# Kernel optimization log

Hardware: AMD Instinct MI355X
Metric: run time of the kernel (lower is better)

## Reference

```python
import jax, jax.numpy as jnp
import numpy as np

KS = 7       # neighborhood kernel size (fixed in __init__)
HEADS = 8    # num_heads (fixed in __init__)
LN_EPS = 1e-5


def _nbr_idx(L, k):
    # NATTEN-style clamped window: window start shifts inward at borders (no padding)
    starts = jnp.clip(jnp.arange(L) - k // 2, 0, L - k)
    idx = starts[:, None] + jnp.arange(k)            # [L, k] absolute neighbor coords
    rel = idx - jnp.arange(L)[:, None] + (k - 1)     # [L, k] rel-pos-bias index in [0, 2k-2]
    return idx, rel


def _na2d(x, qkv_w, qkv_b, proj_w, proj_b, rpb):
    # x: [B, H, W, C]  -> neighborhood attention with clamped 7x7 windows
    B, H, W, C = x.shape
    hd = C // HEADS
    qkv = x @ qkv_w.T + qkv_b                        # [B,H,W,3C]
    q, k, v = jnp.split(qkv, 3, axis=-1)
    q = q.reshape(B, H, W, HEADS, hd) * (hd ** -0.5)
    k = k.reshape(B, H, W, HEADS, hd)
    v = v.reshape(B, H, W, HEADS, hd)
    ri, rri = _nbr_idx(H, KS)                        # [H,KS]
    ci, rci = _nbr_idx(W, KS)                        # [W,KS]
    # gather neighborhoods: [B,H,W,KS,KS,heads,hd]
    kn = k[:, ri[:, None, :, None], ci[None, :, None, :]]
    vn = v[:, ri[:, None, :, None], ci[None, :, None, :]]
    scores = jnp.einsum('bijhd,bijpqhd->bhijpq', q, kn)   # [B,heads,H,W,KS,KS]
    bias = rpb[:, rri[:, None, :, None], rci[None, :, None, :]]  # [heads,H,W,KS,KS]
    scores = scores + bias[None]
    attn = jax.nn.softmax(scores.reshape(B, HEADS, H, W, KS * KS), axis=-1)
    vn = vn.reshape(B, H, W, KS * KS, HEADS, hd)
    out = jnp.einsum('bhijp,bijphd->bijhd', attn, vn)      # [B,H,W,heads,hd]
    out = out.reshape(B, H, W, C)
    return out @ proj_w.T + proj_b


def _layernorm(x, g, b):
    mu = jnp.mean(x, axis=-1, keepdims=True)
    var = jnp.mean((x - mu) ** 2, axis=-1, keepdims=True)
    return (x - mu) * jax.lax.rsqrt(var + LN_EPS) * g + b


def setup_inputs() -> dict:
    key = jax.random.key(0)
    ks = jax.random.split(key, 4)
    B, T, H, W, C = 2, 8, 48, 48, 64
    return {
        'q': jax.random.normal(ks[0], (B, T, H, W, C), dtype=jnp.float32),
        'qkv_w': jax.random.normal(ks[1], (3 * C, C), dtype=jnp.float32) * 0.02,
        'qkv_b': jnp.zeros((3 * C,), jnp.float32),
        'proj_w': jax.random.normal(ks[2], (C, C), dtype=jnp.float32) * 0.02,
        'proj_b': jnp.zeros((C,), jnp.float32),
        'rpb': jax.random.normal(ks[3], (HEADS, 2 * KS - 1, 2 * KS - 1), dtype=jnp.float32) * 0.02,
        'ln_g': jnp.ones((C,), jnp.float32),
        'ln_b': jnp.zeros((C,), jnp.float32),
    }


def reference(q, qkv_w, qkv_b, proj_w, proj_b, rpb, ln_g, ln_b):
    B, T, H, W, C = q.shape
    x = q.reshape(B * T, H, W, C)                    # '(b t) h w c'
    x = _na2d(x, qkv_w, qkv_b, proj_w, proj_b, rpb)  # wPT path
    x = x.reshape(B, T, H, W, C)
    return _layernorm(x, ln_g, ln_b)                 # norm_q; wGC=False
```

## Files before the change

### kernel.cpp

```cpp
#include <hip/hip_runtime.h>
#include <hip/hip_bf16.h>

#define BT   16
#define IH   48
#define IW   48
#define CH   64
#define NH   8
#define HD   8
#define KS   7
#define NPIX (BT*IH*IW)
#define QKVC 192
#define LN_EPS 1e-5f
#define QSCALE 0.35355339059327373f

#define TS   8
#define HS   14
#define HP   (HS*HS)
#define KVS  136
#define AOS  72
#define RPBN (NH*(2*KS-1)*(2*KS-1))

typedef __bf16 bf16_t;
typedef bf16_t bf16x8 __attribute__((ext_vector_type(8)));
typedef float  f32x4  __attribute__((ext_vector_type(4)));

__device__ __forceinline__ float bflo(unsigned u) { union { unsigned i; float f; } v; v.i = u << 16; return v.f; }
__device__ __forceinline__ float bfhi(unsigned u) { union { unsigned i; float f; } v; v.i = u & 0xffff0000u; return v.f; }

__device__ __forceinline__ void ld8bf(const __hip_bfloat16* p, float f[8]) {
    uint4 u = *reinterpret_cast<const uint4*>(p);
    f[0] = bflo(u.x); f[1] = bfhi(u.x);
    f[2] = bflo(u.y); f[3] = bfhi(u.y);
    f[4] = bflo(u.z); f[5] = bfhi(u.z);
    f[6] = bflo(u.w); f[7] = bfhi(u.w);
}

__device__ __forceinline__ void unp8(uint4 u, float f[8]) {
    f[0] = bflo(u.x); f[1] = bfhi(u.x);
    f[2] = bflo(u.y); f[3] = bfhi(u.y);
    f[4] = bflo(u.z); f[5] = bfhi(u.z);
    f[6] = bflo(u.w); f[7] = bfhi(u.w);
}

__device__ __forceinline__ bf16x8 pack_bf16x8(float4 lo, float4 hi) {
    bf16x8 r;
    r[0] = (bf16_t)lo.x; r[1] = (bf16_t)lo.y; r[2] = (bf16_t)lo.z; r[3] = (bf16_t)lo.w;
    r[4] = (bf16_t)hi.x; r[5] = (bf16_t)hi.y; r[6] = (bf16_t)hi.z; r[7] = (bf16_t)hi.w;
    return r;
}

__global__ __launch_bounds__(256) void qkv_kernel(
        const float* __restrict__ x,
        const float* __restrict__ w,
        const float* __restrict__ b,
        __hip_bfloat16* __restrict__ qkv) {
    const int gw   = blockIdx.x * 4 + (threadIdx.x >> 6);
    const int ngrp = gw % 3;
    const int mg   = gw / 3;
    const int l  = threadIdx.x & 63;
    const int m  = l & 15;
    const int kg = l >> 4;

    const int ch_base = ngrp * 64 + m * 4;
    const float4 bias4 = *(const float4*)(b + ch_base);
    const float scale = (ngrp == 0) ? QSCALE : 1.f;

    bf16x8 wb0[4], wb1[4];
    #pragma unroll
    for (int t = 0; t < 4; ++t) {
        const float* wr_ = w + (size_t)(ch_base + t) * CH + kg * 8;
        wb0[t] = pack_bf16x8(*(const float4*)(wr_),      *(const float4*)(wr_ + 4));
        wb1[t] = pack_bf16x8(*(const float4*)(wr_ + 32), *(const float4*)(wr_ + 36));
    }

    #pragma unroll
    for (int mm = 0; mm < 2; ++mm) {
        const int mtile = mg * 2 + mm;
        const float* xr = x + (size_t)(mtile * 16 + m) * CH + kg * 8;
        const bf16x8 a0 = pack_bf16x8(*(const float4*)(xr),      *(const float4*)(xr + 4));
        const bf16x8 a1 = pack_bf16x8(*(const float4*)(xr + 32), *(const float4*)(xr + 36));

        float val[4][4];
        #pragma unroll
        for (int t = 0; t < 4; ++t) {
            f32x4 acc = {0.f, 0.f, 0.f, 0.f};
            acc = __builtin_amdgcn_mfma_f32_16x16x32_bf16(a0, wb0[t], acc, 0, 0, 0);
            acc = __builtin_amdgcn_mfma_f32_16x16x32_bf16(a1, wb1[t], acc, 0, 0, 0);
            const float bias = (t == 0) ? bias4.x : (t == 1) ? bias4.y : (t == 2) ? bias4.z : bias4.w;
            #pragma unroll
            for (int r = 0; r < 4; ++r) val[t][r] = (acc[r] + bias) * scale;
        }
        #pragma unroll
        for (int r = 0; r < 4; ++r) {
            const int pix = mtile * 16 + kg * 4 + r;
            union { ushort4 u; __hip_bfloat16 hh[4]; } pk;
            #pragma unroll
            for (int t = 0; t < 4; ++t) pk.hh[t] = __float2bfloat16(val[t][r]);
            *reinterpret_cast<ushort4*>(qkv + (size_t)pix * QKVC + ch_base) = pk.u;
        }
    }
}

__global__ __launch_bounds__(512, 4) void attn_proj_ln_kernel(
        const __hip_bfloat16* __restrict__ qkv,
        const float* __restrict__ rpb,
        const float* __restrict__ pw,
        const float* __restrict__ pb,
        const float* __restrict__ g,
        const float* __restrict__ beta,
        float* __restrict__ out) {
    __shared__ __align__(16) __hip_bfloat16 kv[HP * KVS];
    __shared__ __align__(16) __hip_bfloat16 ao[TS * TS * AOS];
    __shared__ float rpbs[RPBN];

    const int blk = blockIdx.x;
    const int n   = blk / 36;
    const int t2  = blk % 36;
    const int i0  = (t2 / 6) * TS;
    const int j0  = (t2 % 6) * TS;
    const int tid = threadIdx.x;
    const size_t img = (size_t)n * (IH * IW);

    for (int idx = tid; idx < RPBN; idx += 512) rpbs[idx] = rpb[idx];
    for (int c = tid; c < HP * 16; c += 512) {
        const int px = c >> 4, part = c & 15;
        const int hr = px / HS, hc = px - hr * HS;
        int gr = i0 - 3 + hr; gr = gr < 0 ? 0 : (gr > IH - 1 ? IH - 1 : gr);
        int gc = j0 - 3 + hc; gc = gc < 0 ? 0 : (gc > IW - 1 ? IW - 1 : gc);
        const uint4 v = *reinterpret_cast<const uint4*>(
            qkv + (img + gr * IW + gc) * QKVC + CH + part * 8);
        *reinterpret_cast<uint4*>(kv + px * KVS + part * 8) = v;
    }
    __syncthreads();

    {
        const int h  = tid & 7;
        const int pl = tid >> 3;
        const int i  = i0 + (pl >> 3);
        const int j  = j0 + (pl & 7);

        float qv[HD];
        ld8bf(qkv + (img + i * IW + j) * QKVC + h * HD, qv);

        int si = i - 3; si = si < 0 ? 0 : (si > IH - KS ? IH - KS : si);
        int sj = j - 3; sj = sj < 0 ? 0 : (sj > IW - KS ? IW - KS : sj);
        const float* rp = rpbs + h * (2*KS-1) * (2*KS-1) + (sj - j + (KS - 1));
        const int hjb = sj - (j0 - 3);

        float lrun = 0.f;
        float acc[HD];
        #pragma unroll
        for (int d = 0; d < HD; ++d) acc[d] = 0.f;

        for (int p = 0; p < KS; ++p) {
            const int ki = si + p;
            const float* rprow = rp + (ki - i + (KS - 1)) * (2*KS-1);
            const __hip_bfloat16* row = kv + ((ki - (i0 - 3)) * HS + hjb) * KVS + h * HD;

            uint4 kb[KS], vb[KS];
            #pragma unroll
            for (int qq = 0; qq < KS; ++qq) {
                kb[qq] = *reinterpret_cast<const uint4*>(row + qq * KVS);
                vb[qq] = *reinterpret_cast<const uint4*>(row + qq * KVS + CH);
            }
            float e[KS];
            #pragma unroll
            for (int qq = 0; qq < KS; ++qq) {
                float kf[HD];
                unp8(kb[qq], kf);
                float sc = rprow[qq];
                #pragma unroll
                for (int d = 0; d < HD; ++d) sc += qv[d] * kf[d];
                e[qq] = __expf(sc);
            }
            #pragma unroll
            for (int qq = 0; qq < KS; ++qq) {
                lrun += e[qq];
                float vf[HD];
                unp8(vb[qq], vf);
                #pragma unroll
                for (int d = 0; d < HD; ++d) acc[d] += e[qq] * vf[d];
            }
        }
        const float inv = 1.f / lrun;
        union { uint4 u; __hip_bfloat16 hh[8]; } pk;
        #pragma unroll
        for (int d = 0; d < HD; ++d) pk.hh[d] = __float2bfloat16(acc[d] * inv);
        *reinterpret_cast<uint4*>(ao + pl * AOS + h * HD) = pk.u;
    }
    __syncthreads();

    const int wv = tid >> 6;
    if (wv < 4) {
        const int l  = tid & 63;
        const int m  = l & 15;
        const int kg = l >> 4;

        const __hip_bfloat16* ar = ao + (wv * 16 + m) * AOS + kg * 8;
        const bf16x8 a0 = *reinterpret_cast<const bf16x8*>(ar);
        const bf16x8 a1 = *reinterpret_cast<const bf16x8*>(ar + 32);

        const int ch_base = m * 4;
        const float4 bias4 = *(const float4*)(pb + ch_base);

        float val[4][4];
        #pragma unroll
        for (int t = 0; t < 4; ++t) {
            const float* wr_ = pw + (size_t)(ch_base + t) * CH + kg * 8;
            const bf16x8 b0 = pack_bf16x8(*(const float4*)(wr_),      *(const float4*)(wr_ + 4));
            const bf16x8 b1 = pack_bf16x8(*(const float4*)(wr_ + 32), *(const float4*)(wr_ + 36));
            f32x4 acc = {0.f, 0.f, 0.f, 0.f};
            acc = __builtin_amdgcn_mfma_f32_16x16x32_bf16(a0, b0, acc, 0, 0, 0);
            acc = __builtin_amdgcn_mfma_f32_16x16x32_bf16(a1, b1, acc, 0, 0, 0);
            const float bias = (t == 0) ? bias4.x : (t == 1) ? bias4.y : (t == 2) ? bias4.z : bias4.w;
            #pragma unroll
            for (int r = 0; r < 4; ++r) val[t][r] = acc[r] + bias;
        }

        float sm[4];
        #pragma unroll
        for (int r = 0; r < 4; ++r) sm[r] = val[0][r] + val[1][r] + val[2][r] + val[3][r];
        #pragma unroll
        for (int mask = 1; mask <= 8; mask <<= 1) {
            #pragma unroll
            for (int r = 0; r < 4; ++r) sm[r] += __shfl_xor(sm[r], mask, 64);
        }
        float mu[4];
        #pragma unroll
        for (int r = 0; r < 4; ++r) mu[r] = sm[r] * (1.f / 64.f);

        float qs[4];
        #pragma unroll
        for (int r = 0; r < 4; ++r) {
            float a = val[0][r] - mu[r], bq = val[1][r] - mu[r];
            float c = val[2][r] - mu[r], d = val[3][r] - mu[r];
            qs[r] = a * a + bq * bq + c * c + d * d;
        }
        #pragma unroll
        for (int mask = 1; mask <= 8; mask <<= 1) {
            #pragma unroll
            for (int r = 0; r < 4; ++r) qs[r] += __shfl_xor(qs[r], mask, 64);
        }
        float rs[4];
        #pragma unroll
        for (int r = 0; r < 4; ++r) rs[r] = rsqrtf(qs[r] * (1.f / 64.f) + LN_EPS);

        const float4 g4  = *(const float4*)(g + ch_base);
        const float4 be4 = *(const float4*)(beta + ch_base);
        #pragma unroll
        for (int r = 0; r < 4; ++r) {
            const int pl = wv * 16 + kg * 4 + r;
            const int gi = i0 + (pl >> 3), gj = j0 + (pl & 7);
            float4 o;
            o.x = (val[0][r] - mu[r]) * rs[r] * g4.x + be4.x;
            o.y = (val[1][r] - mu[r]) * rs[r] * g4.y + be4.y;
            o.z = (val[2][r] - mu[r]) * rs[r] * g4.z + be4.z;
            o.w = (val[3][r] - mu[r]) * rs[r] * g4.w + be4.w;
            *reinterpret_cast<float4*>(out + (img + gi * IW + gj) * CH + ch_base) = o;
        }
    }
}

extern "C" void kernel_launch(void* const* d_in, const int* in_sizes, int n_in,
                              void* d_out, int out_size, void* d_ws, size_t ws_size,
                              hipStream_t stream) {
    const float* x      = (const float*)d_in[0];
    const float* qkv_w  = (const float*)d_in[1];
    const float* qkv_b  = (const float*)d_in[2];
    const float* proj_w = (const float*)d_in[3];
    const float* proj_b = (const float*)d_in[4];
    const float* rpb    = (const float*)d_in[5];
    const float* ln_g   = (const float*)d_in[6];
    const float* ln_b   = (const float*)d_in[7];
    float* out = (float*)d_out;

    __hip_bfloat16* qkv = (__hip_bfloat16*)d_ws;

    qkv_kernel<<<864, 256, 0, stream>>>(x, qkv_w, qkv_b, qkv);
    attn_proj_ln_kernel<<<576, 512, 0, stream>>>(qkv, rpb, proj_w, proj_b,
                                                 ln_g, ln_b, out);
}
```

Before: 120.3 us.

## Split fused attention+proj+LN into separate kernels reading K/V directly from global

The fused attention/projection/layernorm kernel becomes two kernels. The attention kernel drops the LDS halo staging and reads K/V and the relative-position bias straight from global memory (through cache), using 256-thread 4x8 tiles and packed f32x2 math. A separate proj+LN kernel reads a bf16 intermediate from the workspace. This removes the LDS footprint and barriers to raise occupancy, at the cost of an extra kernel launch, an intermediate round-trip through memory, and uncached-in-LDS repeated neighbor loads.

After: 120.8 us. About the same (+0.4%).

```diff
diff --git a/kernel.cpp b/kernel.cpp
--- a/kernel.cpp
+++ b/kernel.cpp
@@ -13,34 +13,14 @@
 #define LN_EPS 1e-5f
 #define QSCALE 0.35355339059327373f
 
-#define TS   8
-#define HS   14
-#define HP   (HS*HS)
-#define KVS  136
-#define AOS  72
-#define RPBN (NH*(2*KS-1)*(2*KS-1))
-
 typedef __bf16 bf16_t;
 typedef bf16_t bf16x8 __attribute__((ext_vector_type(8)));
 typedef float  f32x4  __attribute__((ext_vector_type(4)));
+typedef float  f32x2  __attribute__((ext_vector_type(2)));
 
 __device__ __forceinline__ float bflo(unsigned u) { union { unsigned i; float f; } v; v.i = u << 16; return v.f; }
 __device__ __forceinline__ float bfhi(unsigned u) { union { unsigned i; float f; } v; v.i = u & 0xffff0000u; return v.f; }
-
-__device__ __forceinline__ void ld8bf(const __hip_bfloat16* p, float f[8]) {
-    uint4 u = *reinterpret_cast<const uint4*>(p);
-    f[0] = bflo(u.x); f[1] = bfhi(u.x);
-    f[2] = bflo(u.y); f[3] = bfhi(u.y);
-    f[4] = bflo(u.z); f[5] = bfhi(u.z);
-    f[6] = bflo(u.w); f[7] = bfhi(u.w);
-}
-
-__device__ __forceinline__ void unp8(uint4 u, float f[8]) {
-    f[0] = bflo(u.x); f[1] = bfhi(u.x);
-    f[2] = bflo(u.y); f[3] = bfhi(u.y);
-    f[4] = bflo(u.z); f[5] = bfhi(u.z);
-    f[6] = bflo(u.w); f[7] = bfhi(u.w);
-}
+__device__ __forceinline__ f32x2 unp2(unsigned u) { f32x2 r; r.x = bflo(u); r.y = bfhi(u); return r; }
 
 __device__ __forceinline__ bf16x8 pack_bf16x8(float4 lo, float4 hi) {
     bf16x8 r;
@@ -101,163 +81,154 @@
     }
 }
 
-__global__ __launch_bounds__(512, 4) void attn_proj_ln_kernel(
+__global__ __launch_bounds__(256, 8) void attn_kernel(
         const __hip_bfloat16* __restrict__ qkv,
         const float* __restrict__ rpb,
+        __hip_bfloat16* __restrict__ aout) {
+    const int blk  = blockIdx.x;
+    const int n    = blk & 15;
+    const int tile = blk >> 4;
+    const int i0   = (tile / 6) * 4;
+    const int j0   = (tile % 6) * 8;
+    const int tid  = threadIdx.x;
+    const int h    = tid & 7;
+    const int pl   = tid >> 3;
+    const int i    = i0 + (pl >> 3);
+    const int j    = j0 + (pl & 7);
+    const size_t img = (size_t)n * (IH * IW);
+
+    f32x2 qv[4];
+    {
+        const uint4 u = *reinterpret_cast<const uint4*>(
+            qkv + (img + i * IW + j) * QKVC + h * HD);
+        qv[0] = unp2(u.x); qv[1] = unp2(u.y); qv[2] = unp2(u.z); qv[3] = unp2(u.w);
+    }
+
+    int si = i - 3; si = si < 0 ? 0 : (si > IH - KS ? IH - KS : si);
+    int sj = j - 3; sj = sj < 0 ? 0 : (sj > IW - KS ? IW - KS : sj);
+    const float* rp = rpb + h * (2*KS-1) * (2*KS-1) + (sj - j + (KS - 1));
+
+    float lrun = 0.f;
+    f32x2 acc[4];
+    #pragma unroll
+    for (int d = 0; d < 4; ++d) acc[d] = (f32x2){0.f, 0.f};
+
+    for (int p = 0; p < KS; ++p) {
+        const int ki = si + p;
+        const float* rprow = rp + (ki - i + (KS - 1)) * (2*KS-1);
+        const __hip_bfloat16* row = qkv + (img + ki * IW + sj) * QKVC + CH + h * HD;
+
+        uint4 kb[KS];
+        float rb[KS];
+        #pragma unroll
+        for (int qq = 0; qq < KS; ++qq) {
+            kb[qq] = *reinterpret_cast<const uint4*>(row + qq * QKVC);
+            rb[qq] = rprow[qq];
+        }
+        float e[KS];
+        #pragma unroll
+        for (int qq = 0; qq < KS; ++qq) {
+            f32x2 s2 = qv[0] * unp2(kb[qq].x);
+            s2 += qv[1] * unp2(kb[qq].y);
+            s2 += qv[2] * unp2(kb[qq].z);
+            s2 += qv[3] * unp2(kb[qq].w);
+            e[qq] = __expf(s2.x + s2.y + rb[qq]);
+        }
+        uint4 vb[KS];
+        #pragma unroll
+        for (int qq = 0; qq < KS; ++qq)
+            vb[qq] = *reinterpret_cast<const uint4*>(row + qq * QKVC + CH);
+        #pragma unroll
+        for (int qq = 0; qq < KS; ++qq) {
+            lrun += e[qq];
+            acc[0] += e[qq] * unp2(vb[qq].x);
+            acc[1] += e[qq] * unp2(vb[qq].y);
+            acc[2] += e[qq] * unp2(vb[qq].z);
+            acc[3] += e[qq] * unp2(vb[qq].w);
+        }
+    }
+    const float inv = 1.f / lrun;
+    union { uint4 u; __hip_bfloat16 hh[8]; } pk;
+    #pragma unroll
+    for (int d = 0; d < 4; ++d) {
+        pk.hh[2*d]   = __float2bfloat16(acc[d].x * inv);
+        pk.hh[2*d+1] = __float2bfloat16(acc[d].y * inv);
+    }
+    *reinterpret_cast<uint4*>(aout + (img + i * IW + j) * CH + h * HD) = pk.u;
+}
+
+__global__ __launch_bounds__(256) void proj_ln_kernel(
+        const __hip_bfloat16* __restrict__ aout,
         const float* __restrict__ pw,
         const float* __restrict__ pb,
         const float* __restrict__ g,
         const float* __restrict__ beta,
         float* __restrict__ out) {
-    __shared__ __align__(16) __hip_bfloat16 kv[HP * KVS];
-    __shared__ __align__(16) __hip_bfloat16 ao[TS * TS * AOS];
-    __shared__ float rpbs[RPBN];
-
-    const int blk = blockIdx.x;
-    const int n   = blk / 36;
-    const int t2  = blk % 36;
-    const int i0  = (t2 / 6) * TS;
-    const int j0  = (t2 % 6) * TS;
-    const int tid = threadIdx.x;
-    const size_t img = (size_t)n * (IH * IW);
-
-    for (int idx = tid; idx < RPBN; idx += 512) rpbs[idx] = rpb[idx];
-    for (int c = tid; c < HP * 16; c += 512) {
-        const int px = c >> 4, part = c & 15;
-        const int hr = px / HS, hc = px - hr * HS;
-        int gr = i0 - 3 + hr; gr = gr < 0 ? 0 : (gr > IH - 1 ? IH - 1 : gr);
-        int gc = j0 - 3 + hc; gc = gc < 0 ? 0 : (gc > IW - 1 ? IW - 1 : gc);
-        const uint4 v = *reinterpret_cast<const uint4*>(
-            qkv + (img + gr * IW + gc) * QKVC + CH + part * 8);
-        *reinterpret_cast<uint4*>(kv + px * KVS + part * 8) = v;
-    }
-    __syncthreads();
-
-    {
-        const int h  = tid & 7;
-        const int pl = tid >> 3;
-        const int i  = i0 + (pl >> 3);
-        const int j  = j0 + (pl & 7);
-
-        float qv[HD];
-        ld8bf(qkv + (img + i * IW + j) * QKVC + h * HD, qv);
-
-        int si = i - 3; si = si < 0 ? 0 : (si > IH - KS ? IH - KS : si);
-        int sj = j - 3; sj = sj < 0 ? 0 : (sj > IW - KS ? IW - KS : sj);
-        const float* rp = rpbs + h * (2*KS-1) * (2*KS-1) + (sj - j + (KS - 1));
-        const int hjb = sj - (j0 - 3);
-
-        float lrun = 0.f;
-        float acc[HD];
-        #pragma unroll
-        for (int d = 0; d < HD; ++d) acc[d] = 0.f;
-
-        for (int p = 0; p < KS; ++p) {
-            const int ki = si + p;
-            const float* rprow = rp + (ki - i + (KS - 1)) * (2*KS-1);
-            const __hip_bfloat16* row = kv + ((ki - (i0 - 3)) * HS + hjb) * KVS + h * HD;
-
-            uint4 kb[KS], vb[KS];
-            #pragma unroll
-            for (int qq = 0; qq < KS; ++qq) {
-                kb[qq] = *reinterpret_cast<const uint4*>(row + qq * KVS);
-                vb[qq] = *reinterpret_cast<const uint4*>(row + qq * KVS + CH);
-            }
-            float e[KS];
-            #pragma unroll
-            for (int qq = 0; qq < KS; ++qq) {
-                float kf[HD];
-                unp8(kb[qq], kf);
-                float sc = rprow[qq];
-                #pragma unroll
-                for (int d = 0; d < HD; ++d) sc += qv[d] * kf[d];
-                e[qq] = __expf(sc);
-            }
-            #pragma unroll
-            for (int qq = 0; qq < KS; ++qq) {
-                lrun += e[qq];
-                float vf[HD];
-                unp8(vb[qq], vf);
-                #pragma unroll
-                for (int d = 0; d < HD; ++d) acc[d] += e[qq] * vf[d];
-            }
-        }
-        const float inv = 1.f / lrun;
-        union { uint4 u; __hip_bfloat16 hh[8]; } pk;
-        #pragma unroll
-        for (int d = 0; d < HD; ++d) pk.hh[d] = __float2bfloat16(acc[d] * inv);
-        *reinterpret_cast<uint4*>(ao + pl * AOS + h * HD) = pk.u;
-    }
-    __syncthreads();
-
-    const int wv = tid >> 6;
-    if (wv < 4) {
-        const int l  = tid & 63;
-        const int m  = l & 15;
-        const int kg = l >> 4;
-
-        const __hip_bfloat16* ar = ao + (wv * 16 + m) * AOS + kg * 8;
-        const bf16x8 a0 = *reinterpret_cast<const bf16x8*>(ar);
-        const bf16x8 a1 = *reinterpret_cast<const bf16x8*>(ar + 32);
-
-        const int ch_base = m * 4;
-        const float4 bias4 = *(const float4*)(pb + ch_base);
-
-        float val[4][4];
-        #pragma unroll
-        for (int t = 0; t < 4; ++t) {
-            const float* wr_ = pw + (size_t)(ch_base + t) * CH + kg * 8;
-            const bf16x8 b0 = pack_bf16x8(*(const float4*)(wr_),      *(const float4*)(wr_ + 4));
-            const bf16x8 b1 = pack_bf16x8(*(const float4*)(wr_ + 32), *(const float4*)(wr_ + 36));
-            f32x4 acc = {0.f, 0.f, 0.f, 0.f};
-            acc = __builtin_amdgcn_mfma_f32_16x16x32_bf16(a0, b0, acc, 0, 0, 0);
-            acc = __builtin_amdgcn_mfma_f32_16x16x32_bf16(a1, b1, acc, 0, 0, 0);
-            const float bias = (t == 0) ? bias4.x : (t == 1) ? bias4.y : (t == 2) ? bias4.z : bias4.w;
-            #pragma unroll
-            for (int r = 0; r < 4; ++r) val[t][r] = acc[r] + bias;
-        }
-
-        float sm[4];
-        #pragma unroll
-        for (int r = 0; r < 4; ++r) sm[r] = val[0][r] + val[1][r] + val[2][r] + val[3][r];
-        #pragma unroll
-        for (int mask = 1; mask <= 8; mask <<= 1) {
-            #pragma unroll
-            for (int r = 0; r < 4; ++r) sm[r] += __shfl_xor(sm[r], mask, 64);
-        }
-        float mu[4];
-        #pragma unroll
-        for (int r = 0; r < 4; ++r) mu[r] = sm[r] * (1.f / 64.f);
-
-        float qs[4];
-        #pragma unroll
-        for (int r = 0; r < 4; ++r) {
-            float a = val[0][r] - mu[r], bq = val[1][r] - mu[r];
-            float c = val[2][r] - mu[r], d = val[3][r] - mu[r];
-            qs[r] = a * a + bq * bq + c * c + d * d;
-        }
-        #pragma unroll
-        for (int mask = 1; mask <= 8; mask <<= 1) {
-            #pragma unroll
-            for (int r = 0; r < 4; ++r) qs[r] += __shfl_xor(qs[r], mask, 64);
-        }
-        float rs[4];
-        #pragma unroll
-        for (int r = 0; r < 4; ++r) rs[r] = rsqrtf(qs[r] * (1.f / 64.f) + LN_EPS);
-
-        const float4 g4  = *(const float4*)(g + ch_base);
-        const float4 be4 = *(const float4*)(beta + ch_base);
-        #pragma unroll
-        for (int r = 0; r < 4; ++r) {
-            const int pl = wv * 16 + kg * 4 + r;
-            const int gi = i0 + (pl >> 3), gj = j0 + (pl & 7);
-            float4 o;
-            o.x = (val[0][r] - mu[r]) * rs[r] * g4.x + be4.x;
-            o.y = (val[1][r] - mu[r]) * rs[r] * g4.y + be4.y;
-            o.z = (val[2][r] - mu[r]) * rs[r] * g4.z + be4.z;
-            o.w = (val[3][r] - mu[r]) * rs[r] * g4.w + be4.w;
-            *reinterpret_cast<float4*>(out + (img + gi * IW + gj) * CH + ch_base) = o;
-        }
+    const int mtile = (blockIdx.x * blockDim.x + threadIdx.x) >> 6;
+    const int l  = threadIdx.x & 63;
+    const int m  = l & 15;
+    const int kg = l >> 4;
+
+    const __hip_bfloat16* ar = aout + (size_t)(mtile * 16 + m) * CH + kg * 8;
+    const bf16x8 a0 = *reinterpret_cast<const bf16x8*>(ar);
+    const bf16x8 a1 = *reinterpret_cast<const bf16x8*>(ar + 32);
+
+    const int ch_base = m * 4;
+    const float4 bias4 = *(const float4*)(pb + ch_base);
+
+    float val[4][4];
+    #pragma unroll
+    for (int t = 0; t < 4; ++t) {
+        const float* wr_ = pw + (size_t)(ch_base + t) * CH + kg * 8;
+        const bf16x8 b0 = pack_bf16x8(*(const float4*)(wr_),      *(const float4*)(wr_ + 4));
+        const bf16x8 b1 = pack_bf16x8(*(const float4*)(wr_ + 32), *(const float4*)(wr_ + 36));
+        f32x4 acc = {0.f, 0.f, 0.f, 0.f};
+        acc = __builtin_amdgcn_mfma_f32_16x16x32_bf16(a0, b0, acc, 0, 0, 0);
+        acc = __builtin_amdgcn_mfma_f32_16x16x32_bf16(a1, b1, acc, 0, 0, 0);
+        const float bias = (t == 0) ? bias4.x : (t == 1) ? bias4.y : (t == 2) ? bias4.z : bias4.w;
+        #pragma unroll
+        for (int r = 0; r < 4; ++r) val[t][r] = acc[r] + bias;
+    }
+
+    float sm[4];
+    #pragma unroll
+    for (int r = 0; r < 4; ++r) sm[r] = val[0][r] + val[1][r] + val[2][r] + val[3][r];
+    #pragma unroll
+    for (int mask = 1; mask <= 8; mask <<= 1) {
+        #pragma unroll
+        for (int r = 0; r < 4; ++r) sm[r] += __shfl_xor(sm[r], mask, 64);
+    }
+    float mu[4];
+    #pragma unroll
+    for (int r = 0; r < 4; ++r) mu[r] = sm[r] * (1.f / 64.f);
+
+    float qs[4];
+    #pragma unroll
+    for (int r = 0; r < 4; ++r) {
+        float a = val[0][r] - mu[r], bq = val[1][r] - mu[r];
+        float c = val[2][r] - mu[r], d = val[3][r] - mu[r];
+        qs[r] = a * a + bq * bq + c * c + d * d;
+    }
+    #pragma unroll
+    for (int mask = 1; mask <= 8; mask <<= 1) {
+        #pragma unroll
+        for (int r = 0; r < 4; ++r) qs[r] += __shfl_xor(qs[r], mask, 64);
+    }
+    float rs[4];
+    #pragma unroll
+    for (int r = 0; r < 4; ++r) rs[r] = rsqrtf(qs[r] * (1.f / 64.f) + LN_EPS);
+
+    const float4 g4  = *(const float4*)(g + ch_base);
+    const float4 be4 = *(const float4*)(beta + ch_base);
+    #pragma unroll
+    for (int r = 0; r < 4; ++r) {
+        const int pix = mtile * 16 + kg * 4 + r;
+        float4 o;
+        o.x = (val[0][r] - mu[r]) * rs[r] * g4.x + be4.x;
+        o.y = (val[1][r] - mu[r]) * rs[r] * g4.y + be4.y;
+        o.z = (val[2][r] - mu[r]) * rs[r] * g4.z + be4.z;
+        o.w = (val[3][r] - mu[r]) * rs[r] * g4.w + be4.w;
+        *reinterpret_cast<float4*>(out + (size_t)pix * CH + ch_base) = o;
     }
 }
 
@@ -274,9 +245,10 @@
     const float* ln_b   = (const float*)d_in[7];
     float* out = (float*)d_out;
 
-    __hip_bfloat16* qkv = (__hip_bfloat16*)d_ws;
+    __hip_bfloat16* qkv  = (__hip_bfloat16*)d_ws;
+    __hip_bfloat16* aout = (__hip_bfloat16*)((char*)d_ws + (size_t)NPIX * QKVC * 2);
 
     qkv_kernel<<<864, 256, 0, stream>>>(x, qkv_w, qkv_b, qkv);
-    attn_proj_ln_kernel<<<576, 512, 0, stream>>>(qkv, rpb, proj_w, proj_b,
-                                                 ln_g, ln_b, out);
-}
+    attn_kernel<<<1152, 256, 0, stream>>>(qkv, rpb, aout);
+    proj_ln_kernel<<<576, 256, 0, stream>>>(aout, proj_w, proj_b, ln_g, ln_b, out);
+}
```
